# Kernel optimization log

Measured on AMD Instinct MI355X. Metric: run time of the kernel, lower is better.

## Reference

```python
import jax, jax.numpy as jnp
import numpy as np

N_NODES = 50000
N_EDGES = 800000
N_INPUT = 512
N_HIDDEN = 64


def setup_inputs() -> dict:
    key = jax.random.key(0)
    ks = jax.random.split(key, 6)
    x = jax.random.normal(ks[0], (1, N_NODES, N_INPUT), dtype=jnp.float32)
    edge_rows = jax.random.randint(ks[1], (N_EDGES,), 0, N_NODES, dtype=jnp.int64)
    edge_cols = jax.random.randint(ks[2], (N_EDGES,), 0, N_NODES, dtype=jnp.int64)
    edge_vals = jax.random.uniform(ks[3], (N_EDGES,), dtype=jnp.float32)
    # xavier_normal_ on fc.weight: std = sqrt(2 / (fan_in + fan_out))
    std = float(np.sqrt(2.0 / (N_INPUT + N_HIDDEN)))
    W = jax.random.normal(ks[4], (N_HIDDEN, N_INPUT), dtype=jnp.float32) * std
    b = jnp.zeros((N_HIDDEN,), dtype=jnp.float32)
    alpha = jnp.full((1,), 0.25, dtype=jnp.float32)  # PReLU default init
    return {"x": x, "edge_rows": edge_rows, "edge_cols": edge_cols,
            "edge_vals": edge_vals, "W": W, "b": b, "alpha": alpha}


def reference(x, edge_rows, edge_cols, edge_vals, W, b, alpha):
    # Linear projection: [1, N, F_in] @ [F_in, F_out] -> [1, N, F_out]
    h = jnp.einsum('bnf,hf->bnh', x, W) + b
    h = jnp.squeeze(h, 0)  # [N, F_out]
    # spmm(adj, h): out[i] = sum_e vals[e] * h[cols[e]] for rows[e] == i
    msgs = edge_vals[:, None] * h[edge_cols]  # [E, F_out]
    agg = jax.ops.segment_sum(msgs, edge_rows, num_segments=N_NODES)  # [N, F_out]
    out = agg[None, :, :]  # [1, N, F_out]
    # PReLU with shared alpha
    return jnp.where(out >= 0, out, alpha * out)
```

## Files before the change

kernel.cpp:

```cpp
#include <hip/hip_runtime.h>

#define NODES 50000
#define NEDGES 800000
#define NIN 512
#define NHID 64

#define NB 391
#define BCAP 2560
#define EB 4096
#define NBA 196

typedef __attribute__((ext_vector_type(8))) short short8v;
typedef __attribute__((ext_vector_type(8))) unsigned short ushort8v;
typedef __attribute__((ext_vector_type(4))) float f32x4;
typedef __attribute__((ext_vector_type(4))) unsigned int uint4v;

#define H_OFF    0
#define WBF_OFF  1600000
#define GCUR_OFF 1616384
#define RMETA_OFF 1616896
#define ECV2_OFF 1716896

__device__ inline unsigned short f2bf(float f) {
  unsigned u = __builtin_bit_cast(unsigned, f);
  u += 0x7FFF + ((u >> 16) & 1);
  return (unsigned short)(u >> 16);
}
__device__ inline float bf2f(unsigned short u) {
  return __builtin_bit_cast(float, (unsigned)u << 16);
}

__global__ __launch_bounds__(256) void init_kernel(
    const float* __restrict__ W, unsigned int* __restrict__ wbf,
    int* __restrict__ gcur)
{
  int i = blockIdx.x * 256 + threadIdx.x;
  if (i < NIN * NHID / 2) {
    float2 w = reinterpret_cast<const float2*>(W)[i];
    wbf[i] = (unsigned)f2bf(w.x) | ((unsigned)f2bf(w.y) << 16);
  }
  if (i < NB) gcur[i] = 0;
}

__global__ __launch_bounds__(256) void binA_kernel(
    const int* __restrict__ rows, const int* __restrict__ cols,
    const float* __restrict__ vals, int* __restrict__ gcur,
    int2* __restrict__ ecv2)
{
  __shared__ int hist[NB];
  __shared__ unsigned short slots[EB];
  int bid = blockIdx.x;
  int tid = (int)threadIdx.x;
  int e0 = bid * EB;

  for (int i = tid; i < NB; i += 256) hist[i] = 0;
  __syncthreads();
  #pragma unroll 4
  for (int k = 0; k < EB / 256; ++k) {
    int i = e0 + k * 256 + tid;
    if (i < NEDGES) {
      int r = rows[i];
      int s = atomicAdd(&hist[r >> 7], 1);
      slots[k * 256 + tid] = (unsigned short)s;
    }
  }
  __syncthreads();
  for (int i = tid; i < NB; i += 256) {
    int c = hist[i];
    hist[i] = c ? atomicAdd(&gcur[i], c) : 0;
  }
  __syncthreads();
  #pragma unroll 4
  for (int k = 0; k < EB / 256; ++k) {
    int i = e0 + k * 256 + tid;
    if (i < NEDGES) {
      int r = rows[i];
      int bkt = r >> 7;
      int sl = hist[bkt] + (int)slots[k * 256 + tid];
      if (sl < BCAP)
        ecv2[(long)bkt * BCAP + sl] =
            make_int2(cols[i] | ((r & 127) << 17), __float_as_int(vals[i]));
    }
  }
}

__global__ __launch_bounds__(512) void gemm_kernel(
    const float* __restrict__ x, const unsigned short* __restrict__ wbf,
    const float* __restrict__ b, unsigned short* __restrict__ h)
{
  __shared__ float red[8][64][18];
  int blk = blockIdx.x;
  int tid = (int)threadIdx.x;
  int w = tid >> 6;
  int lane = tid & 63;
  int g  = w & 1;
  int kc = w >> 1;
  int r16 = lane & 15;
  int kg  = lane >> 4;

  long row = (long)blk * 32 + g * 16 + r16;
  if (row >= NODES) row = NODES - 1;
  const float* xp = x + row * NIN + kg * 8;
  const unsigned short* wp = wbf + (long)r16 * NIN + kg * 8;

  f32x4 acc[4] = {{0,0,0,0},{0,0,0,0},{0,0,0,0},{0,0,0,0}};

  #pragma unroll
  for (int m = 0; m < 4; ++m) {
    int M = kc * 4 + m;
    float4 a0 = *reinterpret_cast<const float4*>(xp + M * 32);
    float4 a1 = *reinterpret_cast<const float4*>(xp + M * 32 + 4);
    unsigned q0, q1, q2, q3;
    asm("v_cvt_pk_bf16_f32 %0, %1, %2" : "=v"(q0) : "v"(a0.x), "v"(a0.y));
    asm("v_cvt_pk_bf16_f32 %0, %1, %2" : "=v"(q1) : "v"(a0.z), "v"(a0.w));
    asm("v_cvt_pk_bf16_f32 %0, %1, %2" : "=v"(q2) : "v"(a1.x), "v"(a1.y));
    asm("v_cvt_pk_bf16_f32 %0, %1, %2" : "=v"(q3) : "v"(a1.z), "v"(a1.w));
    uint4v ap = {q0, q1, q2, q3};
    short8v af = __builtin_bit_cast(short8v, ap);
    #pragma unroll
    for (int ft = 0; ft < 4; ++ft) {
      short8v bfr = *reinterpret_cast<const short8v*>(
          wp + (long)ft * 16 * NIN + M * 32);
      acc[ft] = __builtin_amdgcn_mfma_f32_16x16x32_bf16(af, bfr, acc[ft], 0, 0, 0);
    }
  }

  #pragma unroll
  for (int ft = 0; ft < 4; ++ft) {
    *reinterpret_cast<float2*>(&red[w][lane][ft * 4]) =
        make_float2(acc[ft][0], acc[ft][1]);
    *reinterpret_cast<float2*>(&red[w][lane][ft * 4 + 2]) =
        make_float2(acc[ft][2], acc[ft][3]);
  }
  __syncthreads();

  #pragma unroll
  for (int j = 0; j < 4; ++j) {
    int o = tid * 4 + j;
    int og  = o >> 10;
    int ol  = (o >> 4) & 63;
    int idx = o & 15;
    float s = red[0 * 2 + og][ol][idx] + red[1 * 2 + og][ol][idx]
            + red[2 * 2 + og][ol][idx] + red[3 * 2 + og][ol][idx];
    int ft = idx >> 2, r = idx & 3;
    int f = ft * 16 + (ol & 15);
    long node = (long)blk * 32 + og * 16 + (ol >> 4) * 4 + r;
    if (node < NODES)
      h[node * NHID + f] = f2bf(s + b[f]);
  }
}

__global__ __launch_bounds__(256) void sortb_kernel(
    const int* __restrict__ gcur, int2* __restrict__ ecv2,
    int2* __restrict__ rowmeta)
{
  __shared__ int2 ed[BCAP];
  __shared__ unsigned short slots[BCAP];
  __shared__ int hist[128], base[128], stmp[128];
  int bkt = blockIdx.x;
  int tid = (int)threadIdx.x;

  int n = gcur[bkt];
  if (n > BCAP) n = BCAP;
  int2* bptr = ecv2 + (long)bkt * BCAP;

  if (tid < 128) hist[tid] = 0;
  __syncthreads();

  for (int i = tid; i < n; i += 256) {
    int2 e = bptr[i];
    ed[i] = e;
    int rl = e.x >> 17;
    slots[i] = (unsigned short)atomicAdd(&hist[rl], 1);
  }
  __syncthreads();

  int v = (tid < 128) ? hist[tid] : 0;
  if (tid < 128) stmp[tid] = v;
  __syncthreads();
  for (int d = 1; d < 128; d <<= 1) {
    int t = (tid < 128 && tid >= d) ? stmp[tid - d] : 0;
    __syncthreads();
    if (tid < 128) stmp[tid] += t;
    __syncthreads();
  }
  if (tid < 128) base[tid] = stmp[tid] - v;
  __syncthreads();

  for (int i = tid; i < n; i += 256) {
    int2 e = ed[i];
    int rl = e.x >> 17;
    int pos = base[rl] + (int)slots[i];
    bptr[pos] = make_int2(e.x & 0x1FFFF, e.y);
  }

  if (tid < 128) {
    int row = bkt * 128 + tid;
    if (row < NODES)
      rowmeta[row] = make_int2(bkt * BCAP + base[tid], hist[tid]);
  }
}

__global__ __launch_bounds__(256) void gather_kernel(
    const int2* __restrict__ rowmeta, const int2* __restrict__ ecv2,
    const unsigned short* __restrict__ h, const float* __restrict__ alpha,
    float* __restrict__ out)
{
  int wid = (int)((blockIdx.x * 256 + threadIdx.x) >> 6);
  if (wid >= NODES) return;
  int lane = (int)(threadIdx.x & 63);
  int eg = lane >> 3;
  int fo = lane & 7;
  int2 m = rowmeta[wid];
  int deg = m.y;
  const int2* base = ecv2 + m.x;
  float a = alpha[0];

  float acc[8] = {0.f, 0.f, 0.f, 0.f, 0.f, 0.f, 0.f, 0.f};
  int j = eg;
  int2 e = (j < deg) ? base[j] : make_int2(0, 0);
  while (j < deg) {
    int2 en = (j + 8 < deg) ? base[j + 8] : make_int2(0, 0);
    float v = __int_as_float(e.y);
    ushort8v hv = *reinterpret_cast<const ushort8v*>(&h[(long)e.x * NHID + fo * 8]);
    #pragma unroll
    for (int k = 0; k < 8; ++k)
      acc[k] = fmaf(v, bf2f(hv[k]), acc[k]);
    e = en;
    j += 8;
  }

  #pragma unroll
  for (int k = 0; k < 8; ++k) {
    acc[k] += __shfl_xor(acc[k], 8);
    acc[k] += __shfl_xor(acc[k], 16);
    acc[k] += __shfl_xor(acc[k], 32);
  }

  if (eg == 0) {
    float4 o0, o1;
    o0.x = acc[0] >= 0.f ? acc[0] : a * acc[0];
    o0.y = acc[1] >= 0.f ? acc[1] : a * acc[1];
    o0.z = acc[2] >= 0.f ? acc[2] : a * acc[2];
    o0.w = acc[3] >= 0.f ? acc[3] : a * acc[3];
    o1.x = acc[4] >= 0.f ? acc[4] : a * acc[4];
    o1.y = acc[5] >= 0.f ? acc[5] : a * acc[5];
    o1.z = acc[6] >= 0.f ? acc[6] : a * acc[6];
    o1.w = acc[7] >= 0.f ? acc[7] : a * acc[7];
    *reinterpret_cast<float4*>(&out[(long)wid * NHID + fo * 8]) = o0;
    *reinterpret_cast<float4*>(&out[(long)wid * NHID + fo * 8 + 4]) = o1;
  }
}

extern "C" void kernel_launch(void* const* d_in, const int* in_sizes, int n_in,
                              void* d_out, int out_size, void* d_ws, size_t ws_size,
                              hipStream_t stream) {
  const float* x     = (const float*)d_in[0];
  const int*   rows  = (const int*)d_in[1];
  const int*   cols  = (const int*)d_in[2];
  const float* vals  = (const float*)d_in[3];
  const float* W     = (const float*)d_in[4];
  const float* b     = (const float*)d_in[5];
  const float* alpha = (const float*)d_in[6];
  float* out = (float*)d_out;

  float* wsf = (float*)d_ws;
  unsigned short* h     = (unsigned short*)(wsf + H_OFF);
  unsigned int*   wbf   = (unsigned int*)(wsf + WBF_OFF);
  int*            gcur  = (int*)(wsf + GCUR_OFF);
  int2*           rmeta = (int2*)(wsf + RMETA_OFF);
  int2*           ecv2  = (int2*)(wsf + ECV2_OFF);

  init_kernel<<<64, 256, 0, stream>>>(W, wbf, gcur);
  binA_kernel<<<NBA, 256, 0, stream>>>(rows, cols, vals, gcur, ecv2);
  gemm_kernel<<<(NODES + 31) / 32, 512, 0, stream>>>(
      x, (const unsigned short*)wbf, b, h);
  sortb_kernel<<<NB, 256, 0, stream>>>(gcur, ecv2, rmeta);
  gather_kernel<<<NODES * 64 / 256, 256, 0, stream>>>(rmeta, ecv2, h, alpha, out);
}
```

Measured before the change: 99.82 us.

## Pre-convert x to bf16 in extra blocks of the binning kernel

Adds a bf16 conversion pass over x, run by extra blocks appended to the edge-binning kernel, writing a bf16 copy of x into the workspace. The GEMM kernel then loads bf16 activations directly instead of loading fp32 and converting in-register. The aim is to overlap the conversion with binning and halve the GEMM's activation load width. In exchange, total memory traffic on x rises: a full fp32 read, a bf16 write, then a bf16 read.

```diff
diff --git a/kernel.cpp b/kernel.cpp
--- a/kernel.cpp
+++ b/kernel.cpp
@@ -9,6 +9,8 @@
 #define BCAP 2560
 #define EB 4096
 #define NBA 196
+#define CVB 2048
+#define NCHUNK 3200000
 
 typedef __attribute__((ext_vector_type(8))) short short8v;
 typedef __attribute__((ext_vector_type(8))) unsigned short ushort8v;
@@ -20,6 +22,7 @@
 #define GCUR_OFF 1616384
 #define RMETA_OFF 1616896
 #define ECV2_OFF 1716896
+#define XBF_OFF  3718816
 
 __device__ inline unsigned short f2bf(float f) {
   unsigned u = __builtin_bit_cast(unsigned, f);
@@ -42,17 +45,34 @@
   if (i < NB) gcur[i] = 0;
 }
 
-__global__ __launch_bounds__(256) void binA_kernel(
+__global__ __launch_bounds__(256) void fat_kernel(
     const int* __restrict__ rows, const int* __restrict__ cols,
     const float* __restrict__ vals, int* __restrict__ gcur,
-    int2* __restrict__ ecv2)
+    int2* __restrict__ ecv2,
+    const float* __restrict__ x, unsigned short* __restrict__ xbf)
 {
   __shared__ int hist[NB];
   __shared__ unsigned short slots[EB];
   int bid = blockIdx.x;
   int tid = (int)threadIdx.x;
+
+  if (bid >= NBA) {
+    uint4v* dst = reinterpret_cast<uint4v*>(xbf);
+    for (int j = (bid - NBA) * 256 + tid; j < NCHUNK; j += CVB * 256) {
+      float4 v0 = *reinterpret_cast<const float4*>(x + (long)j * 8);
+      float4 v1 = *reinterpret_cast<const float4*>(x + (long)j * 8 + 4);
+      unsigned q0, q1, q2, q3;
+      asm("v_cvt_pk_bf16_f32 %0, %1, %2" : "=v"(q0) : "v"(v0.x), "v"(v0.y));
+      asm("v_cvt_pk_bf16_f32 %0, %1, %2" : "=v"(q1) : "v"(v0.z), "v"(v0.w));
+      asm("v_cvt_pk_bf16_f32 %0, %1, %2" : "=v"(q2) : "v"(v1.x), "v"(v1.y));
+      asm("v_cvt_pk_bf16_f32 %0, %1, %2" : "=v"(q3) : "v"(v1.z), "v"(v1.w));
+      uint4v q = {q0, q1, q2, q3};
+      dst[j] = q;
+    }
+    return;
+  }
+
   int e0 = bid * EB;
-
   for (int i = tid; i < NB; i += 256) hist[i] = 0;
   __syncthreads();
   #pragma unroll 4
@@ -85,7 +105,7 @@
 }
 
 __global__ __launch_bounds__(512) void gemm_kernel(
-    const float* __restrict__ x, const unsigned short* __restrict__ wbf,
+    const unsigned short* __restrict__ xbf, const unsigned short* __restrict__ wbf,
     const float* __restrict__ b, unsigned short* __restrict__ h)
 {
   __shared__ float red[8][64][18];
@@ -100,7 +120,7 @@
 
   long row = (long)blk * 32 + g * 16 + r16;
   if (row >= NODES) row = NODES - 1;
-  const float* xp = x + row * NIN + kg * 8;
+  const unsigned short* xp = xbf + row * NIN + kc * 128 + kg * 8;
   const unsigned short* wp = wbf + (long)r16 * NIN + kg * 8;
 
   f32x4 acc[4] = {{0,0,0,0},{0,0,0,0},{0,0,0,0},{0,0,0,0}};
@@ -108,15 +128,7 @@
   #pragma unroll
   for (int m = 0; m < 4; ++m) {
     int M = kc * 4 + m;
-    float4 a0 = *reinterpret_cast<const float4*>(xp + M * 32);
-    float4 a1 = *reinterpret_cast<const float4*>(xp + M * 32 + 4);
-    unsigned q0, q1, q2, q3;
-    asm("v_cvt_pk_bf16_f32 %0, %1, %2" : "=v"(q0) : "v"(a0.x), "v"(a0.y));
-    asm("v_cvt_pk_bf16_f32 %0, %1, %2" : "=v"(q1) : "v"(a0.z), "v"(a0.w));
-    asm("v_cvt_pk_bf16_f32 %0, %1, %2" : "=v"(q2) : "v"(a1.x), "v"(a1.y));
-    asm("v_cvt_pk_bf16_f32 %0, %1, %2" : "=v"(q3) : "v"(a1.z), "v"(a1.w));
-    uint4v ap = {q0, q1, q2, q3};
-    short8v af = __builtin_bit_cast(short8v, ap);
+    short8v af = *reinterpret_cast<const short8v*>(xp + m * 32);
     #pragma unroll
     for (int ft = 0; ft < 4; ++ft) {
       short8v bfr = *reinterpret_cast<const short8v*>(
@@ -270,11 +282,12 @@
   int*            gcur  = (int*)(wsf + GCUR_OFF);
   int2*           rmeta = (int2*)(wsf + RMETA_OFF);
   int2*           ecv2  = (int2*)(wsf + ECV2_OFF);
+  unsigned short* xbf   = (unsigned short*)(wsf + XBF_OFF);
 
   init_kernel<<<64, 256, 0, stream>>>(W, wbf, gcur);
-  binA_kernel<<<NBA, 256, 0, stream>>>(rows, cols, vals, gcur, ecv2);
+  fat_kernel<<<NBA + CVB, 256, 0, stream>>>(rows, cols, vals, gcur, ecv2, x, xbf);
   gemm_kernel<<<(NODES + 31) / 32, 512, 0, stream>>>(
-      x, (const unsigned short*)wbf, b, h);
+      xbf, (const unsigned short*)wbf, b, h);
   sortb_kernel<<<NB, 256, 0, stream>>>(gcur, ecv2, rmeta);
   gather_kernel<<<NODES * 64 / 256, 256, 0, stream>>>(rmeta, ecv2, h, alpha, out);
 }
```

After: 109.2 us. +9.4%, slower.
